# Kernel tuning notes

Hardware: AMD Instinct MI355X
Metric: run time of the kernel (lower is better)

Reference implementation:

```python
import jax, jax.numpy as jnp
import numpy as np

N_NODES = 100000


def gcn_conv(x, W, b, src, dst, n):
    """PyG GCNConv: add self-loops, symmetric normalization, aggregate."""
    x = x @ W  # [N, out]
    loop = jnp.arange(n, dtype=src.dtype)
    src_f = jnp.concatenate([src, loop])  # sources (message origins)
    dst_f = jnp.concatenate([dst, loop])  # targets (aggregation index)
    ones = jnp.ones(src_f.shape[0], dtype=x.dtype)
    deg = jax.ops.segment_sum(ones, dst_f, num_segments=n)
    dinv = jnp.where(deg > 0, jax.lax.rsqrt(deg), 0.0)
    norm = dinv[src_f] * dinv[dst_f]  # [E+N]
    msg = x[src_f] * norm[:, None]  # gather + scale
    out = jax.ops.segment_sum(msg, dst_f, num_segments=n)  # scatter-add
    return out + b


def setup_inputs() -> dict:
    key = jax.random.key(0)
    k1, k2, k3, k4 = jax.random.split(key, 4)
    in_f, hid, ncls = 128, 128, 64
    n_edges = 1600000
    x = jax.random.normal(k1, (N_NODES, in_f), dtype=jnp.float32)
    W1 = jax.random.normal(k2, (in_f, hid), dtype=jnp.float32) * (1.0 / np.sqrt(in_f))
    b1 = jnp.zeros((hid,), dtype=jnp.float32)
    W2 = jax.random.normal(k3, (hid, ncls), dtype=jnp.float32) * (1.0 / np.sqrt(hid))
    b2 = jnp.zeros((ncls,), dtype=jnp.float32)
    edge_index = jax.random.randint(k4, (2, n_edges), 0, N_NODES, dtype=jnp.int32)
    return {"x": x, "W1": W1, "b1": b1, "W2": W2, "b2": b2, "edge_index": edge_index}


def reference(x, W1, b1, W2, b2, edge_index):
    src, dst = edge_index[0], edge_index[1]
    n = x.shape[0]
    h = gcn_conv(x, W1, b1, src, dst, n)
    h = jax.nn.relu(h)
    # dropout p=0.5 is identity in eval mode
    h = gcn_conv(h, W2, b2, src, dst, n)
    return jax.nn.log_softmax(h, axis=1)
```

## Files before the change

### kernel.cpp

```cpp
#include <hip/hip_runtime.h>
#include <math.h>

#define N_NODES 100000
#define N_EDGES 1600000
#define NB 391
#define MROWS 100096
#define CH 3200
#define ZROW N_NODES

typedef __attribute__((ext_vector_type(8))) short short8;
typedef __attribute__((ext_vector_type(4))) float f32x4;
typedef __attribute__((ext_vector_type(2))) float f32x2;

__device__ __forceinline__ short f2b(float f) {
    unsigned u = __float_as_uint(f);
    unsigned r = (u + 0x7FFFu + ((u >> 16) & 1u)) >> 16;
    return (short)r;
}
__device__ __forceinline__ unsigned pk2(float a, float b) {
    return (unsigned)(unsigned short)f2b(a) | ((unsigned)(unsigned short)f2b(b) << 16);
}
__device__ __forceinline__ unsigned char f2q(float v) {
    return (unsigned char)(__builtin_amdgcn_cvt_pk_fp8_f32(v, 0.f, 0, false) & 0xFF);
}
__device__ __forceinline__ void acc4(float* a, unsigned u) {
    f32x2 lo = __builtin_amdgcn_cvt_pk_f32_fp8((int)u, false);
    f32x2 hi = __builtin_amdgcn_cvt_pk_f32_fp8((int)u, true);
    a[0] += lo[0]; a[1] += lo[1]; a[2] += hi[0]; a[3] += hi[1];
}

__device__ __forceinline__ short8 pack8t(const float* __restrict__ p) {
    float4 v0 = ((const float4*)p)[0];
    float4 v1 = ((const float4*)p)[1];
    union { unsigned u[4]; short8 s; } r;
    r.u[0] = __builtin_amdgcn_perm(__float_as_uint(v0.y), __float_as_uint(v0.x), 0x07060302u);
    r.u[1] = __builtin_amdgcn_perm(__float_as_uint(v0.w), __float_as_uint(v0.z), 0x07060302u);
    r.u[2] = __builtin_amdgcn_perm(__float_as_uint(v1.y), __float_as_uint(v1.x), 0x07060302u);
    r.u[3] = __builtin_amdgcn_perm(__float_as_uint(v1.w), __float_as_uint(v1.z), 0x07060302u);
    return r.s;
}

__global__ __launch_bounds__(512) void init_misc(int* __restrict__ bcnt,
                                                 unsigned* __restrict__ y1s,
                                                 unsigned* __restrict__ y2s) {
    int t = threadIdx.x;
    if (t < NB) bcnt[t] = 0;
    if (t < 32) y1s[t] = 0;
    if (t < 16) y2s[t] = 0;
}

__global__ __launch_bounds__(256) void bucket_count(const int* __restrict__ dst,
                                                    int* __restrict__ bcnt) {
    __shared__ int h[NB];
    int t = threadIdx.x;
    for (int i = t; i < NB; i += 256) h[i] = 0;
    __syncthreads();
    for (int e = blockIdx.x * 256 + t; e < N_EDGES; e += gridDim.x * 256)
        atomicAdd(&h[dst[e] >> 8], 1);
    __syncthreads();
    for (int i = t; i < NB; i += 256)
        if (h[i]) atomicAdd(&bcnt[i], h[i]);
}

__global__ __launch_bounds__(512) void bucket_scan(const int* __restrict__ bcnt,
                                                   int* __restrict__ boffs,
                                                   int* __restrict__ bcur) {
    __shared__ int s[512];
    int t = threadIdx.x;
    int v = (t < NB) ? bcnt[t] : 0;
    s[t] = v;
    __syncthreads();
    for (int off = 1; off < 512; off <<= 1) {
        int u = (t >= off) ? s[t - off] : 0;
        __syncthreads();
        s[t] += u;
        __syncthreads();
    }
    if (t < NB) {
        int ex = s[t] - v;
        boffs[t] = ex;
        bcur[t] = ex;
    }
    if (t == 0) boffs[NB] = N_EDGES;
}

__global__ __launch_bounds__(256) void bucket_scatter(const int* __restrict__ src,
                                                      const int* __restrict__ dst,
                                                      int* __restrict__ bcur,
                                                      unsigned* __restrict__ pairs) {
    __shared__ unsigned lw[CH];
    __shared__ short lb[CH];
    __shared__ int cnt[NB];
    __shared__ int lstart[NB];
    int t = threadIdx.x;
    int e0 = blockIdx.x * CH;
    int n = min(CH, N_EDGES - e0);
    for (int i = t; i < NB; i += 256) cnt[i] = 0;
    __syncthreads();
    for (int i = t; i < n; i += 256) {
        int s = src[e0 + i], d = dst[e0 + i];
        lw[i] = ((unsigned)(d & 255) << 24) | (unsigned)s;
        int b = d >> 8;
        lb[i] = (short)b;
        atomicAdd(&cnt[b], 1);
    }
    __syncthreads();
    for (int b = t; b < NB; b += 256) {
        int c = cnt[b];
        lstart[b] = c ? atomicAdd(&bcur[b], c) : 0;
        cnt[b] = 0;
    }
    __syncthreads();
    for (int i = t; i < n; i += 256) {
        int b = lb[i];
        int lo = atomicAdd(&cnt[b], 1);
        pairs[lstart[b] + lo] = lw[i];
    }
}

__global__ __launch_bounds__(256) void csr_fill_bucket(const unsigned* __restrict__ pairs,
                                                       const int* __restrict__ boffs,
                                                       int2* __restrict__ rinfo,
                                                       float* __restrict__ dinv,
                                                       int* __restrict__ srcs) {
    __shared__ int lcnt[256];
    __shared__ int ls[256];
    int t = threadIdx.x, b = blockIdx.x, base = b << 8;
    lcnt[t] = 0;
    __syncthreads();
    int lo_e = boffs[b], hi_e = boffs[b + 1];
    for (int i = lo_e + t; i < hi_e; i += 256)
        atomicAdd(&lcnt[pairs[i] >> 24], 1);
    __syncthreads();
    int c = lcnt[t];
    int cpad = (c + 7) & ~7;
    ls[t] = cpad;
    __syncthreads();
    for (int off = 1; off < 256; off <<= 1) {
        int u = (t >= off) ? ls[t - off] : 0;
        __syncthreads();
        ls[t] += u;
        __syncthreads();
    }
    int pbase = ((lo_e + 7) & ~7) + b * 2048;
    int rp = pbase + ls[t] - cpad;
    int node = base + t;
    if (node < N_NODES) {
        rinfo[node] = make_int2(rp, rp + cpad);
        dinv[node] = rsqrtf((float)(c + 1));
    }
    __syncthreads();
    lcnt[t] = rp;
    __syncthreads();
    for (int i = lo_e + t; i < hi_e; i += 256) {
        unsigned p = pairs[i];
        int li = p >> 24;
        int pos = atomicAdd(&lcnt[li], 1);
        srcs[pos] = (int)(p & 0xFFFFFFu);
    }
    __syncthreads();
    for (int i = lcnt[t], stop = rp + cpad; i < stop; ++i) srcs[i] = ZROW;
}

__global__ __launch_bounds__(256) void convert_w(const float* __restrict__ W1,
                                                 const float* __restrict__ W2,
                                                 short* __restrict__ w1h,
                                                 short* __restrict__ w2h) {
    int id = blockIdx.x * 256 + threadIdx.x;
    if (id < 128 * 128) {
        int n = id >> 7, k = id & 127;
        w1h[id] = f2b(W1[k * 128 + n]);
    } else if (id < 128 * 128 + 64 * 128) {
        int j = id - 128 * 128;
        int n = j >> 7, k = j & 127;
        w2h[j] = f2b(W2[k * 64 + n]);
    }
}

__global__ __launch_bounds__(512) void gemm1_mfma(const float* __restrict__ X,
                                                  const short* __restrict__ Wt,
                                                  const float* __restrict__ dinv,
                                                  unsigned char* __restrict__ Yf) {
    __shared__ short Ws[128 * 128];
    const int t = threadIdx.x;
    for (int i = t * 8; i < 128 * 128; i += 512 * 8)
        *(short8*)(Ws + i) = *(const short8*)(Wt + i);
    __syncthreads();

    const int w = t >> 6, lane = t & 63;
    const int m = lane & 15, q = lane >> 4;
    const int r0 = blockIdx.x * 128 + w * 16;
    const int ra = min(r0 + m, N_NODES - 1);

    f32x4 acc[8];
#pragma unroll
    for (int c = 0; c < 8; ++c) acc[c] = (f32x4)(0.f);

#pragma unroll
    for (int kk = 0; kk < 4; ++kk) {
        const int koff = kk * 32 + q * 8;
        short8 a = pack8t(X + (size_t)ra * 128 + koff);
#pragma unroll
        for (int c = 0; c < 8; ++c) {
            short8 bh = *(const short8*)(Ws + (c * 16 + m) * 128 + koff);
            acc[c] = __builtin_amdgcn_mfma_f32_16x16x32_bf16(a, bh, acc[c], 0, 0, 0);
        }
    }

    const int rb0 = r0 + q * 4;
    f32x4 dv = *(const f32x4*)(dinv + rb0);
#pragma unroll
    for (int c = 0; c < 8; ++c) {
        const int col = c * 16 + m;
#pragma unroll
        for (int r = 0; r < 4; ++r) {
            int row = rb0 + r;
            if (row < N_NODES) Yf[(size_t)row * 128 + col] = f2q(acc[c][r] * dv[r]);
        }
    }
}

__global__ __launch_bounds__(512) void gemm2_mfma(const short* __restrict__ H,
                                                  const short* __restrict__ Wt,
                                                  const float* __restrict__ dinv,
                                                  unsigned char* __restrict__ Yf) {
    __shared__ short Ws[64 * 128];
    const int t = threadIdx.x;
    for (int i = t * 8; i < 64 * 128; i += 512 * 8)
        *(short8*)(Ws + i) = *(const short8*)(Wt + i);
    __syncthreads();

    const int w = t >> 6, lane = t & 63;
    const int m = lane & 15, q = lane >> 4;
    const int r0 = blockIdx.x * 128 + w * 16;

    f32x4 acc[4];
#pragma unroll
    for (int c = 0; c < 4; ++c) acc[c] = (f32x4)(0.f);

#pragma unroll
    for (int kk = 0; kk < 4; ++kk) {
        const int koff = kk * 32 + q * 8;
        short8 a = *(const short8*)(H + (size_t)(r0 + m) * 128 + koff);
#pragma unroll
        for (int c = 0; c < 4; ++c) {
            short8 bh = *(const short8*)(Ws + (c * 16 + m) * 128 + koff);
            acc[c] = __builtin_amdgcn_mfma_f32_16x16x32_bf16(a, bh, acc[c], 0, 0, 0);
        }
    }

    const int rb0 = r0 + q * 4;
    f32x4 dv = *(const f32x4*)(dinv + rb0);
#pragma unroll
    for (int c = 0; c < 4; ++c) {
        const int col = c * 16 + m;
#pragma unroll
        for (int r = 0; r < 4; ++r) {
            int row = rb0 + r;
            if (row < N_NODES) Yf[(size_t)row * 64 + col] = f2q(acc[c][r] * dv[r]);
        }
    }
}

__global__ __launch_bounds__(256) void agg_relu(const int2* __restrict__ rinfo,
                                                const int* __restrict__ srcs,
                                                const unsigned char* __restrict__ Yf,
                                                const float* __restrict__ dinv,
                                                const float* __restrict__ b,
                                                short* __restrict__ Hb) {
    int t = threadIdx.x;
    int lane = t & 63, w = t >> 6;
    int half = lane >> 5, li = lane & 31;
    int d0 = blockIdx.x * 8 + 2 * w;
    int d1 = d0 + 1;
    const unsigned fo = (unsigned)(li << 2);
    int2 r0 = rinfo[d0], r1 = rinfo[d1];
    float a0[4] = {0.f, 0.f, 0.f, 0.f};
    float a1[4] = {0.f, 0.f, 0.f, 0.f};
    {
        unsigned dh = half ? (unsigned)d1 : (unsigned)d0;
        unsigned su = *(const unsigned*)(Yf + ((dh << 7) + fo));
        if (!half) acc4(a0, su); else acc4(a1, su);
    }
    int e0 = r0.x, n0 = r0.y, e1 = r1.x, n1 = r1.y;
    while (true) {
        bool c0 = e0 < n0, c1 = e1 < n1;
        if (!(c0 | c1)) break;
        if (c0) {
            uint4 s = *(const uint4*)(srcs + e0 + 4 * half);
            unsigned g0 = *(const unsigned*)(Yf + (((unsigned)s.x << 7) + fo));
            unsigned g1 = *(const unsigned*)(Yf + (((unsigned)s.y << 7) + fo));
            unsigned g2 = *(const unsigned*)(Yf + (((unsigned)s.z << 7) + fo));
            unsigned g3 = *(const unsigned*)(Yf + (((unsigned)s.w << 7) + fo));
            acc4(a0, g0); acc4(a0, g1); acc4(a0, g2); acc4(a0, g3);
            e0 += 8;
        }
        if (c1) {
            uint4 s = *(const uint4*)(srcs + e1 + 4 * half);
            unsigned g0 = *(const unsigned*)(Yf + (((unsigned)s.x << 7) + fo));
            unsigned g1 = *(const unsigned*)(Yf + (((unsigned)s.y << 7) + fo));
            unsigned g2 = *(const unsigned*)(Yf + (((unsigned)s.z << 7) + fo));
            unsigned g3 = *(const unsigned*)(Yf + (((unsigned)s.w << 7) + fo));
            acc4(a1, g0); acc4(a1, g1); acc4(a1, g2); acc4(a1, g3);
            e1 += 8;
        }
    }
#pragma unroll
    for (int i = 0; i < 4; ++i) {
        a0[i] += __shfl_xor(a0[i], 32);
        a1[i] += __shfl_xor(a1[i], 32);
    }
    int dd = half ? d1 : d0;
    float s0 = half ? a1[0] : a0[0];
    float s1 = half ? a1[1] : a0[1];
    float s2 = half ? a1[2] : a0[2];
    float s3 = half ? a1[3] : a0[3];
    float sc = dinv[dd];
    float4 bb = ((const float4*)b)[li];
    float v0 = fmaxf(sc * s0 + bb.x, 0.f);
    float v1 = fmaxf(sc * s1 + bb.y, 0.f);
    float v2 = fmaxf(sc * s2 + bb.z, 0.f);
    float v3 = fmaxf(sc * s3 + bb.w, 0.f);
    ((uint2*)Hb)[(size_t)dd * 32 + li] = make_uint2(pk2(v0, v1), pk2(v2, v3));
}

__global__ __launch_bounds__(256) void agg_lsm(const int2* __restrict__ rinfo,
                                               const int* __restrict__ srcs,
                                               const unsigned char* __restrict__ Yf,
                                               const float* __restrict__ dinv,
                                               const float* __restrict__ b,
                                               float* __restrict__ out) {
    int t = threadIdx.x;
    int lane = t & 63, w = t >> 6;
    int gi = lane >> 4, li = lane & 15;
    int d0 = blockIdx.x * 8 + 2 * w;
    int d1 = d0 + 1;
    const unsigned fo = (unsigned)(li << 2);
    int2 r0 = rinfo[d0], r1 = rinfo[d1];
    float a0[4] = {0.f, 0.f, 0.f, 0.f};
    float a1[4] = {0.f, 0.f, 0.f, 0.f};
    {
        unsigned dh = (gi == 1) ? (unsigned)d1 : (unsigned)d0;
        unsigned su = *(const unsigned*)(Yf + ((dh << 6) + fo));
        if (gi == 0) acc4(a0, su);
        else if (gi == 1) acc4(a1, su);
    }
    int e0 = r0.x, n0 = r0.y, e1 = r1.x, n1 = r1.y;
    while (true) {
        bool c0 = e0 < n0, c1 = e1 < n1;
        if (!(c0 | c1)) break;
        if (c0) {
            uint2 s = *(const uint2*)(srcs + e0 + 2 * gi);
            unsigned g0 = *(const unsigned*)(Yf + (((unsigned)s.x << 6) + fo));
            unsigned g1 = *(const unsigned*)(Yf + (((unsigned)s.y << 6) + fo));
            acc4(a0, g0); acc4(a0, g1);
            e0 += 8;
        }
        if (c1) {
            uint2 s = *(const uint2*)(srcs + e1 + 2 * gi);
            unsigned g0 = *(const unsigned*)(Yf + (((unsigned)s.x << 6) + fo));
            unsigned g1 = *(const unsigned*)(Yf + (((unsigned)s.y << 6) + fo));
            acc4(a1, g0); acc4(a1, g1);
            e1 += 8;
        }
    }
#pragma unroll
    for (int i = 0; i < 4; ++i) {
        a0[i] += __shfl_xor(a0[i], 16);
        a0[i] += __shfl_xor(a0[i], 32);
        a1[i] += __shfl_xor(a1[i], 16);
        a1[i] += __shfl_xor(a1[i], 32);
    }
    int gsel = gi >> 1;
    int dd = gsel ? d1 : d0;
    float s0 = gsel ? a1[0] : a0[0];
    float s1 = gsel ? a1[1] : a0[1];
    float s2 = gsel ? a1[2] : a0[2];
    float s3 = gsel ? a1[3] : a0[3];
    float sc = dinv[dd];
    float4 bb = ((const float4*)b)[li];
    float v0 = sc * s0 + bb.x;
    float v1 = sc * s1 + bb.y;
    float v2 = sc * s2 + bb.z;
    float v3 = sc * s3 + bb.w;
    float m = fmaxf(fmaxf(v0, v1), fmaxf(v2, v3));
#pragma unroll
    for (int o = 1; o <= 8; o <<= 1) m = fmaxf(m, __shfl_xor(m, o));
    float su = __expf(v0 - m) + __expf(v1 - m) + __expf(v2 - m) + __expf(v3 - m);
#pragma unroll
    for (int o = 1; o <= 8; o <<= 1) su += __shfl_xor(su, o);
    float ls = m + logf(su);
    if ((gi & 1) == 0)
        ((float4*)out)[(size_t)dd * 16 + li] =
            make_float4(v0 - ls, v1 - ls, v2 - ls, v3 - ls);
}

extern "C" void kernel_launch(void* const* d_in, const int* in_sizes, int n_in,
                              void* d_out, int out_size, void* d_ws, size_t ws_size,
                              hipStream_t stream) {
    const float* x  = (const float*)d_in[0];
    const float* W1 = (const float*)d_in[1];
    const float* b1 = (const float*)d_in[2];
    const float* W2 = (const float*)d_in[3];
    const float* b2 = (const float*)d_in[4];
    const int* edge = (const int*)d_in[5];
    const int* src = edge;
    const int* dst = edge + N_EDGES;
    float* out = (float*)d_out;

    char* ws = (char*)d_ws;
    int*           bcnt  = (int*)(ws + 0);
    int*           boffs = (int*)(ws + 2048);
    int*           bcur  = (int*)(ws + 4096);
    float*         dinv  = (float*)(ws + 6144);
    int2*          rinfo = (int2*)(ws + 406528);
    int*           srcs  = (int*)(ws + 1206528);
    unsigned*      pairs = (unsigned*)(ws + 14012672);
    short*         w1h   = (short*)(ws + 20412672);
    short*         w2h   = (short*)(ws + 20445440);
    unsigned char* y1f   = (unsigned char*)(ws + 20461824);
    short*         h1b   = (short*)(ws + 33274112);
    unsigned char* y2f   = (unsigned char*)(ws + 58898688);

    init_misc<<<1, 512, 0, stream>>>(bcnt,
                                     (unsigned*)(y1f + (size_t)N_NODES * 128),
                                     (unsigned*)(y2f + (size_t)N_NODES * 64));

    bucket_count<<<512, 256, 0, stream>>>(dst, bcnt);
    bucket_scan<<<1, 512, 0, stream>>>(bcnt, boffs, bcur);
    bucket_scatter<<<(N_EDGES + CH - 1) / CH, 256, 0, stream>>>(src, dst, bcur, pairs);
    csr_fill_bucket<<<NB, 256, 0, stream>>>(pairs, boffs, rinfo, dinv, srcs);

    convert_w<<<(128 * 128 + 64 * 128 + 255) / 256, 256, 0, stream>>>(W1, W2, w1h, w2h);

    gemm1_mfma<<<MROWS / 128, 512, 0, stream>>>(x, w1h, dinv, y1f);
    agg_relu<<<N_NODES / 8, 256, 0, stream>>>(rinfo, srcs, y1f, dinv, b1, h1b);

    gemm2_mfma<<<MROWS / 128, 512, 0, stream>>>(h1b, w2h, dinv, y2f);
    agg_lsm<<<N_NODES / 8, 256, 0, stream>>>(rinfo, srcs, y2f, dinv, b2, out);
}
```

Baseline: 269.0 us.

## Fold self-loop into CSR and software-pipeline index loads in aggregation kernels

The CSR fill now stores each node's own index as the first entry of its row, with padding grown by one slot, so the aggregation kernels no longer need a separate self-loop gather. The aggregation loops are restructured to prefetch the next chunk of source indices while the current feature gathers are in flight, and they accumulate with packed two-float vector adds. The goal is to hide index-load latency behind the gathers and remove divergent self-loop code, at the cost of a slightly larger index array and more live registers.

```diff
diff --git a/kernel.cpp b/kernel.cpp
--- a/kernel.cpp
+++ b/kernel.cpp
@@ -23,10 +23,9 @@
 __device__ __forceinline__ unsigned char f2q(float v) {
     return (unsigned char)(__builtin_amdgcn_cvt_pk_fp8_f32(v, 0.f, 0, false) & 0xFF);
 }
-__device__ __forceinline__ void acc4(float* a, unsigned u) {
-    f32x2 lo = __builtin_amdgcn_cvt_pk_f32_fp8((int)u, false);
-    f32x2 hi = __builtin_amdgcn_cvt_pk_f32_fp8((int)u, true);
-    a[0] += lo[0]; a[1] += lo[1]; a[2] += hi[0]; a[3] += hi[1];
+__device__ __forceinline__ void acc2(f32x2* a, unsigned u) {
+    a[0] += __builtin_amdgcn_cvt_pk_f32_fp8((int)u, false);
+    a[1] += __builtin_amdgcn_cvt_pk_f32_fp8((int)u, true);
 }
 
 __device__ __forceinline__ short8 pack8t(const float* __restrict__ p) {
@@ -133,7 +132,7 @@
         atomicAdd(&lcnt[pairs[i] >> 24], 1);
     __syncthreads();
     int c = lcnt[t];
-    int cpad = (c + 7) & ~7;
+    int cpad = (c + 8) & ~7;
     ls[t] = cpad;
     __syncthreads();
     for (int off = 1; off < 256; off <<= 1) {
@@ -142,15 +141,16 @@
         ls[t] += u;
         __syncthreads();
     }
-    int pbase = ((lo_e + 7) & ~7) + b * 2048;
+    int pbase = ((lo_e + 7) & ~7) + b * 2056;
     int rp = pbase + ls[t] - cpad;
     int node = base + t;
     if (node < N_NODES) {
         rinfo[node] = make_int2(rp, rp + cpad);
         dinv[node] = rsqrtf((float)(c + 1));
-    }
-    __syncthreads();
-    lcnt[t] = rp;
+        srcs[rp] = node;
+    }
+    __syncthreads();
+    lcnt[t] = rp + 1;
     __syncthreads();
     for (int i = lo_e + t; i < hi_e; i += 256) {
         unsigned p = pairs[i];
@@ -275,52 +275,54 @@
     int d1 = d0 + 1;
     const unsigned fo = (unsigned)(li << 2);
     int2 r0 = rinfo[d0], r1 = rinfo[d1];
-    float a0[4] = {0.f, 0.f, 0.f, 0.f};
-    float a1[4] = {0.f, 0.f, 0.f, 0.f};
-    {
-        unsigned dh = half ? (unsigned)d1 : (unsigned)d0;
-        unsigned su = *(const unsigned*)(Yf + ((dh << 7) + fo));
-        if (!half) acc4(a0, su); else acc4(a1, su);
-    }
+    f32x2 a0[2] = {(f32x2)(0.f), (f32x2)(0.f)};
+    f32x2 a1[2] = {(f32x2)(0.f), (f32x2)(0.f)};
     int e0 = r0.x, n0 = r0.y, e1 = r1.x, n1 = r1.y;
-    while (true) {
-        bool c0 = e0 < n0, c1 = e1 < n1;
+    uint4 s0 = *(const uint4*)(srcs + e0 + 4 * half);
+    uint4 s1 = *(const uint4*)(srcs + e1 + 4 * half);
+    bool c0 = true, c1 = true;
+    for (;;) {
+        bool p0 = c0, p1 = c1;
+        unsigned g00, g01, g02, g03, g10, g11, g12, g13;
+        if (p0) {
+            g00 = *(const unsigned*)(Yf + (((unsigned)s0.x << 7) + fo));
+            g01 = *(const unsigned*)(Yf + (((unsigned)s0.y << 7) + fo));
+            g02 = *(const unsigned*)(Yf + (((unsigned)s0.z << 7) + fo));
+            g03 = *(const unsigned*)(Yf + (((unsigned)s0.w << 7) + fo));
+            e0 += 8;
+            c0 = e0 < n0;
+        }
+        if (p1) {
+            g10 = *(const unsigned*)(Yf + (((unsigned)s1.x << 7) + fo));
+            g11 = *(const unsigned*)(Yf + (((unsigned)s1.y << 7) + fo));
+            g12 = *(const unsigned*)(Yf + (((unsigned)s1.z << 7) + fo));
+            g13 = *(const unsigned*)(Yf + (((unsigned)s1.w << 7) + fo));
+            e1 += 8;
+            c1 = e1 < n1;
+        }
+        if (c0) s0 = *(const uint4*)(srcs + e0 + 4 * half);
+        if (c1) s1 = *(const uint4*)(srcs + e1 + 4 * half);
+        if (p0) { acc2(a0, g00); acc2(a0, g01); acc2(a0, g02); acc2(a0, g03); }
+        if (p1) { acc2(a1, g10); acc2(a1, g11); acc2(a1, g12); acc2(a1, g13); }
         if (!(c0 | c1)) break;
-        if (c0) {
-            uint4 s = *(const uint4*)(srcs + e0 + 4 * half);
-            unsigned g0 = *(const unsigned*)(Yf + (((unsigned)s.x << 7) + fo));
-            unsigned g1 = *(const unsigned*)(Yf + (((unsigned)s.y << 7) + fo));
-            unsigned g2 = *(const unsigned*)(Yf + (((unsigned)s.z << 7) + fo));
-            unsigned g3 = *(const unsigned*)(Yf + (((unsigned)s.w << 7) + fo));
-            acc4(a0, g0); acc4(a0, g1); acc4(a0, g2); acc4(a0, g3);
-            e0 += 8;
-        }
-        if (c1) {
-            uint4 s = *(const uint4*)(srcs + e1 + 4 * half);
-            unsigned g0 = *(const unsigned*)(Yf + (((unsigned)s.x << 7) + fo));
-            unsigned g1 = *(const unsigned*)(Yf + (((unsigned)s.y << 7) + fo));
-            unsigned g2 = *(const unsigned*)(Yf + (((unsigned)s.z << 7) + fo));
-            unsigned g3 = *(const unsigned*)(Yf + (((unsigned)s.w << 7) + fo));
-            acc4(a1, g0); acc4(a1, g1); acc4(a1, g2); acc4(a1, g3);
-            e1 += 8;
-        }
-    }
-#pragma unroll
-    for (int i = 0; i < 4; ++i) {
-        a0[i] += __shfl_xor(a0[i], 32);
-        a1[i] += __shfl_xor(a1[i], 32);
-    }
+    }
+    float t00 = a0[0][0], t01 = a0[0][1], t02 = a0[1][0], t03 = a0[1][1];
+    float t10 = a1[0][0], t11 = a1[0][1], t12 = a1[1][0], t13 = a1[1][1];
+    t00 += __shfl_xor(t00, 32); t01 += __shfl_xor(t01, 32);
+    t02 += __shfl_xor(t02, 32); t03 += __shfl_xor(t03, 32);
+    t10 += __shfl_xor(t10, 32); t11 += __shfl_xor(t11, 32);
+    t12 += __shfl_xor(t12, 32); t13 += __shfl_xor(t13, 32);
     int dd = half ? d1 : d0;
-    float s0 = half ? a1[0] : a0[0];
-    float s1 = half ? a1[1] : a0[1];
-    float s2 = half ? a1[2] : a0[2];
-    float s3 = half ? a1[3] : a0[3];
+    float s0f = half ? t10 : t00;
+    float s1f = half ? t11 : t01;
+    float s2f = half ? t12 : t02;
+    float s3f = half ? t13 : t03;
     float sc = dinv[dd];
     float4 bb = ((const float4*)b)[li];
-    float v0 = fmaxf(sc * s0 + bb.x, 0.f);
-    float v1 = fmaxf(sc * s1 + bb.y, 0.f);
-    float v2 = fmaxf(sc * s2 + bb.z, 0.f);
-    float v3 = fmaxf(sc * s3 + bb.w, 0.f);
+    float v0 = fmaxf(sc * s0f + bb.x, 0.f);
+    float v1 = fmaxf(sc * s1f + bb.y, 0.f);
+    float v2 = fmaxf(sc * s2f + bb.z, 0.f);
+    float v3 = fmaxf(sc * s3f + bb.w, 0.f);
     ((uint2*)Hb)[(size_t)dd * 32 + li] = make_uint2(pk2(v0, v1), pk2(v2, v3));
 }
 
@@ -337,52 +339,55 @@
     int d1 = d0 + 1;
     const unsigned fo = (unsigned)(li << 2);
     int2 r0 = rinfo[d0], r1 = rinfo[d1];
-    float a0[4] = {0.f, 0.f, 0.f, 0.f};
-    float a1[4] = {0.f, 0.f, 0.f, 0.f};
-    {
-        unsigned dh = (gi == 1) ? (unsigned)d1 : (unsigned)d0;
-        unsigned su = *(const unsigned*)(Yf + ((dh << 6) + fo));
-        if (gi == 0) acc4(a0, su);
-        else if (gi == 1) acc4(a1, su);
-    }
+    f32x2 a0[2] = {(f32x2)(0.f), (f32x2)(0.f)};
+    f32x2 a1[2] = {(f32x2)(0.f), (f32x2)(0.f)};
     int e0 = r0.x, n0 = r0.y, e1 = r1.x, n1 = r1.y;
-    while (true) {
-        bool c0 = e0 < n0, c1 = e1 < n1;
+    uint2 s0 = *(const uint2*)(srcs + e0 + 2 * gi);
+    uint2 s1 = *(const uint2*)(srcs + e1 + 2 * gi);
+    bool c0 = true, c1 = true;
+    for (;;) {
+        bool p0 = c0, p1 = c1;
+        unsigned g00, g01, g10, g11;
+        if (p0) {
+            g00 = *(const unsigned*)(Yf + (((unsigned)s0.x << 6) + fo));
+            g01 = *(const unsigned*)(Yf + (((unsigned)s0.y << 6) + fo));
+            e0 += 8;
+            c0 = e0 < n0;
+        }
+        if (p1) {
+            g10 = *(const unsigned*)(Yf + (((unsigned)s1.x << 6) + fo));
+            g11 = *(const unsigned*)(Yf + (((unsigned)s1.y << 6) + fo));
+            e1 += 8;
+            c1 = e1 < n1;
+        }
+        if (c0) s0 = *(const uint2*)(srcs + e0 + 2 * gi);
+        if (c1) s1 = *(const uint2*)(srcs + e1 + 2 * gi);
+        if (p0) { acc2(a0, g00); acc2(a0, g01); }
+        if (p1) { acc2(a1, g10); acc2(a1, g11); }
         if (!(c0 | c1)) break;
-        if (c0) {
-            uint2 s = *(const uint2*)(srcs + e0 + 2 * gi);
-            unsigned g0 = *(const unsigned*)(Yf + (((unsigned)s.x << 6) + fo));
-            unsigned g1 = *(const unsigned*)(Yf + (((unsigned)s.y << 6) + fo));
-            acc4(a0, g0); acc4(a0, g1);
-            e0 += 8;
-        }
-        if (c1) {
-            uint2 s = *(const uint2*)(srcs + e1 + 2 * gi);
-            unsigned g0 = *(const unsigned*)(Yf + (((unsigned)s.x << 6) + fo));
-            unsigned g1 = *(const unsigned*)(Yf + (((unsigned)s.y << 6) + fo));
-            acc4(a1, g0); acc4(a1, g1);
-            e1 += 8;
-        }
-    }
-#pragma unroll
-    for (int i = 0; i < 4; ++i) {
-        a0[i] += __shfl_xor(a0[i], 16);
-        a0[i] += __shfl_xor(a0[i], 32);
-        a1[i] += __shfl_xor(a1[i], 16);
-        a1[i] += __shfl_xor(a1[i], 32);
-    }
+    }
+    float t00 = a0[0][0], t01 = a0[0][1], t02 = a0[1][0], t03 = a0[1][1];
+    float t10 = a1[0][0], t11 = a1[0][1], t12 = a1[1][0], t13 = a1[1][1];
+    t00 += __shfl_xor(t00, 16); t00 += __shfl_xor(t00, 32);
+    t01 += __shfl_xor(t01, 16); t01 += __shfl_xor(t01, 32);
+    t02 += __shfl_xor(t02, 16); t02 += __shfl_xor(t02, 32);
+    t03 += __shfl_xor(t03, 16); t03 += __shfl_xor(t03, 32);
+    t10 += __shfl_xor(t10, 16); t10 += __shfl_xor(t10, 32);
+    t11 += __shfl_xor(t11, 16); t11 += __shfl_xor(t11, 32);
+    t12 += __shfl_xor(t12, 16); t12 += __shfl_xor(t12, 32);
+    t13 += __shfl_xor(t13, 16); t13 += __shfl_xor(t13, 32);
     int gsel = gi >> 1;
     int dd = gsel ? d1 : d0;
-    float s0 = gsel ? a1[0] : a0[0];
-    float s1 = gsel ? a1[1] : a0[1];
-    float s2 = gsel ? a1[2] : a0[2];
-    float s3 = gsel ? a1[3] : a0[3];
+    float s0f = gsel ? t10 : t00;
+    float s1f = gsel ? t11 : t01;
+    float s2f = gsel ? t12 : t02;
+    float s3f = gsel ? t13 : t03;
     float sc = dinv[dd];
     float4 bb = ((const float4*)b)[li];
-    float v0 = sc * s0 + bb.x;
-    float v1 = sc * s1 + bb.y;
-    float v2 = sc * s2 + bb.z;
-    float v3 = sc * s3 + bb.w;
+    float v0 = sc * s0f + bb.x;
+    float v1 = sc * s1f + bb.y;
+    float v2 = sc * s2f + bb.z;
+    float v3 = sc * s3f + bb.w;
     float m = fmaxf(fmaxf(v0, v1), fmaxf(v2, v3));
 #pragma unroll
     for (int o = 1; o <= 8; o <<= 1) m = fmaxf(m, __shfl_xor(m, o));
```

Result: faster. 262.8 us (-2.3%).
